# Kernel optimization log

Measured on AMD Instinct MI355X. Metric: run time of the kernel, lower is better.

Reference implementation:

```python
import jax, jax.numpy as jnp
import numpy as np

BN_EPS = 1e-5

def setup_inputs() -> dict:
    key = jax.random.key(0)
    ks = jax.random.split(key, 8)
    N, E, D = 50000, 800000, 128
    x = jax.random.normal(ks[0], (N, D), dtype=jnp.float32)
    edge_index = jax.random.randint(ks[1], (2, E), 0, N, dtype=jnp.int64)
    s = 1.0 / np.sqrt(D)
    W1 = jax.random.uniform(ks[2], (D, D), jnp.float32, -s, s)
    b1 = jax.random.uniform(ks[3], (D,), jnp.float32, -s, s)
    W2 = jax.random.uniform(ks[4], (D, D), jnp.float32, -s, s)
    b2 = jax.random.uniform(ks[5], (D,), jnp.float32, -s, s)
    g1 = jnp.ones((D,), jnp.float32); be1 = jnp.zeros((D,), jnp.float32)
    g2 = jnp.ones((D,), jnp.float32); be2 = jnp.zeros((D,), jnp.float32)
    eps = jnp.zeros((), jnp.float32)  # learnable GIN epsilon (train_eps=True)
    return {"x": x, "edge_index": edge_index, "eps": eps,
            "W1": W1, "b1": b1, "g1": g1, "be1": be1,
            "W2": W2, "b2": b2, "g2": g2, "be2": be2}

def _batchnorm(h, gamma, beta):
    # training-mode BatchNorm1d over node axis (biased variance)
    mu = jnp.mean(h, axis=0)
    var = jnp.mean(jnp.square(h - mu), axis=0)
    return (h - mu) * jax.lax.rsqrt(var + BN_EPS) * gamma + beta

def reference(x, edge_index, eps, W1, b1, g1, be1, W2, b2, g2, be2):
    N = x.shape[0]
    src, dst = edge_index[0], edge_index[1]
    # GIN aggregation: sum of neighbor features (scatter-add to target nodes)
    agg = jax.ops.segment_sum(x[src], dst, num_segments=N)  # [N, D]
    h = (1.0 + eps) * x + agg
    # MLP: Linear -> BN -> ReLU -> Linear
    h = h @ W1.T + b1
    h = jax.nn.relu(_batchnorm(h, g1, be1))
    h = h @ W2.T + b2
    # outer BatchNorm + ReLU
    return jax.nn.relu(_batchnorm(h, g2, be2))
```

## Files before the change

### kernel.cpp

```cpp
#include <hip/hip_runtime.h>
#include <hip/hip_bf16.h>


#define DIM 128
#define SUB 2
#define CAP 32
#define KMAX 64
#define RBLK 2048

typedef unsigned short u16;
typedef __attribute__((ext_vector_type(8))) short short8;
typedef __attribute__((ext_vector_type(8))) unsigned short ushort8;
typedef __attribute__((ext_vector_type(4))) float f32x4;

__device__ inline u16 f2b(float f) {
  unsigned int u = __builtin_bit_cast(unsigned int, f);
  u += 0x7fffu + ((u >> 16) & 1u);
  return (u16)(u >> 16);
}
__device__ inline float b2f(u16 b) {
  unsigned int u = ((unsigned int)b) << 16;
  return __builtin_bit_cast(float, u);
}

__global__ __launch_bounds__(256) void setup_kernel(
    const float* __restrict__ W1, const float* __restrict__ W2,
    int* __restrict__ cursor, u16* __restrict__ wb1, u16* __restrict__ wb2, int ZC) {
  int i = blockIdx.x * 256 + threadIdx.x;
  const int stride = gridDim.x * 256;
  const int e1 = ZC + 4096, e2 = ZC + 8192;
  for (; i < e2; i += stride) {
    if (i < ZC) {
      int4 z = {0, 0, 0, 0};
      reinterpret_cast<int4*>(cursor)[i] = z;
    } else if (i < e1) {
      const int j = i - ZC;
      const float4 v = reinterpret_cast<const float4*>(W1)[j];
      ushort4 o = {f2b(v.x), f2b(v.y), f2b(v.z), f2b(v.w)};
      reinterpret_cast<ushort4*>(wb1)[j] = o;
    } else {
      const int j = i - e1;
      const float4 v = reinterpret_cast<const float4*>(W2)[j];
      ushort4 o = {f2b(v.x), f2b(v.y), f2b(v.z), f2b(v.w)};
      reinterpret_cast<ushort4*>(wb2)[j] = o;
    }
  }
}

__global__ __launch_bounds__(256) void reorder_gemmy_kernel(
    const float* __restrict__ x, const int* __restrict__ ei, const u16* __restrict__ wb1,
    int* __restrict__ cursor, u16* __restrict__ buckets, u16* __restrict__ yb,
    int E, float p8N, int N, int GB) {
  const int bid = blockIdx.x;
  if (bid < GB) {
    const int lane = threadIdx.x & 63;
    const int wid = threadIdx.x >> 6;
    const int l15 = lane & 15;
    const int lg = lane >> 4;
    const int wrow = bid * 64 + wid * 16;

    f32x4 acc[8];
#pragma unroll
    for (int ni = 0; ni < 8; ++ni) acc[ni] = (f32x4){0.f, 0.f, 0.f, 0.f};

    int arow = wrow + l15;
    if (arow >= N) arow = N - 1;

#pragma unroll
    for (int kb = 0; kb < 4; ++kb) {
      const int k0 = kb * 32 + lg * 8;
      const f32x4* A = reinterpret_cast<const f32x4*>(x + (size_t)arow * DIM + k0);
      const f32x4 v0 = __builtin_nontemporal_load(A);
      const f32x4 v1 = __builtin_nontemporal_load(A + 1);
      short8 a;
      a[0] = (short)f2b(v0.x); a[1] = (short)f2b(v0.y);
      a[2] = (short)f2b(v0.z); a[3] = (short)f2b(v0.w);
      a[4] = (short)f2b(v1.x); a[5] = (short)f2b(v1.y);
      a[6] = (short)f2b(v1.z); a[7] = (short)f2b(v1.w);
#pragma unroll
      for (int ni = 0; ni < 8; ++ni) {
        const short8 b = *reinterpret_cast<const short8*>(wb1 + (ni * 16 + l15) * DIM + k0);
        acc[ni] = __builtin_amdgcn_mfma_f32_16x16x32_bf16(a, b, acc[ni], 0, 0, 0);
      }
    }
    const int rbase = wrow + lg * 4;
#pragma unroll
    for (int ni = 0; ni < 8; ++ni) {
      const int col = ni * 16 + l15;
#pragma unroll
      for (int r = 0; r < 4; ++r) {
        const int row = rbase + r;
        if (row < N) yb[(size_t)row * DIM + col] = f2b(acc[ni][r]);
      }
    }
  } else {
    const int rb = bid - GB;
    const int part = rb & 7;
    const int slice = rb >> 3;
    const int perE = (E + 255) >> 8;
    const int beg = slice * perE;
    const int end = min(E, beg + perE);
    const int way = threadIdx.x & 1;
    for (int e = beg + (int)threadIdx.x; e < end; e += 256) {
      const int d = __builtin_nontemporal_load(ei + E + e);
      int p = (int)((float)d * p8N);
      if (p > 7) p = 7;
      if (p != part) continue;
      const int s = __builtin_nontemporal_load(ei + e);
      const int pos = atomicAdd(&cursor[d * SUB + way], 1);
      if (pos < CAP) buckets[d * KMAX + way * CAP + pos] = (u16)s;
    }
  }
}

__global__ __launch_bounds__(256) void aggregate_kernel(
    const u16* __restrict__ yb, const int* __restrict__ cursor,
    const u16* __restrict__ buckets, const float* __restrict__ epsp,
    const float* __restrict__ b1, float* __restrict__ h1, int N) {
  const int wid = threadIdx.x >> 6;
  const int lane = threadIdx.x & 63;
  const int node = blockIdx.x * 4 + wid;
  if (node >= N) return;
  const int slot = lane >> 4;
  const int chunk = lane & 15;
  int c0 = cursor[node * SUB + 0]; if (c0 > CAP) c0 = CAP;
  int c1 = cursor[node * SUB + 1]; if (c1 > CAP) c1 = CAP;
  const int deg = c0 + c1;
  const u16* bk = buckets + node * KMAX;

  int my = 0;
  if (lane < c0) my = bk[lane];
  else if (lane - c0 < c1) my = bk[CAP + lane - c0];

  float acc[8];
#pragma unroll
  for (int f = 0; f < 8; ++f) acc[f] = 0.f;

  for (int t0 = 0; t0 < deg; t0 += 8) {
    const int i1 = t0 + slot;
    const int i2 = t0 + 4 + slot;
    const int s1 = __shfl(my, i1);
    const int s2 = __shfl(my, i2);
    const ushort8 v1 = *reinterpret_cast<const ushort8*>(yb + (size_t)s1 * DIM + chunk * 8);
    const ushort8 v2 = *reinterpret_cast<const ushort8*>(yb + (size_t)s2 * DIM + chunk * 8);
    if (i1 < deg) {
#pragma unroll
      for (int f = 0; f < 8; ++f) acc[f] += b2f(v1[f]);
    }
    if (i2 < deg) {
#pragma unroll
      for (int f = 0; f < 8; ++f) acc[f] += b2f(v2[f]);
    }
  }
#pragma unroll
  for (int f = 0; f < 8; ++f) {
    acc[f] += __shfl_xor(acc[f], 16);
    acc[f] += __shfl_xor(acc[f], 32);
  }
  if (slot == 0) {
    const float k = 1.0f + epsp[0];
    const ushort8 xv = *reinterpret_cast<const ushort8*>(yb + (size_t)node * DIM + chunk * 8);
    const float4 bb0 = *reinterpret_cast<const float4*>(b1 + chunk * 8);
    const float4 bb1 = *reinterpret_cast<const float4*>(b1 + chunk * 8 + 4);
    float4 o0, o1;
    o0.x = acc[0] + k * b2f(xv[0]) + bb0.x;
    o0.y = acc[1] + k * b2f(xv[1]) + bb0.y;
    o0.z = acc[2] + k * b2f(xv[2]) + bb0.z;
    o0.w = acc[3] + k * b2f(xv[3]) + bb0.w;
    o1.x = acc[4] + k * b2f(xv[4]) + bb1.x;
    o1.y = acc[5] + k * b2f(xv[5]) + bb1.y;
    o1.z = acc[6] + k * b2f(xv[6]) + bb1.z;
    o1.w = acc[7] + k * b2f(xv[7]) + bb1.w;
    float4* dst = reinterpret_cast<float4*>(h1 + (size_t)node * DIM + chunk * 8);
    dst[0] = o0;
    dst[1] = o1;
  }
}

__global__ __launch_bounds__(256) void stats_kernel(
    const float* __restrict__ H, float* __restrict__ stats, int N) {
  __shared__ float red[256];
  const int col = threadIdx.x & 127;
  const int sub = threadIdx.x >> 7;
  float s = 0.f, sq = 0.f;
  for (int row = blockIdx.x * 2 + sub; row < N; row += gridDim.x * 2) {
    const float v = H[(size_t)row * DIM + col];
    s += v;
    sq = fmaf(v, v, sq);
  }
  red[threadIdx.x] = s;
  __syncthreads();
  if (sub == 0) unsafeAtomicAdd(&stats[col], s + red[threadIdx.x + 128]);
  __syncthreads();
  red[threadIdx.x] = sq;
  __syncthreads();
  if (sub == 0) unsafeAtomicAdd(&stats[DIM + col], sq + red[threadIdx.x + 128]);
}

__global__ __launch_bounds__(256) void gemm2_kernel(
    const float* __restrict__ A, const u16* __restrict__ Wb,
    const float* __restrict__ bias, const float* __restrict__ statsIn,
    const float* __restrict__ gamma, const float* __restrict__ beta,
    u16* __restrict__ C, float* __restrict__ statsOut, int N, float Ninv) {
  __shared__ float sred[4][DIM];
  __shared__ float qred[4][DIM];
  __shared__ float ssc[DIM];
  __shared__ float ssh[DIM];
  {
    const int t = threadIdx.x;
    if (t < DIM) {
      const float mu = statsIn[t] * Ninv;
      const float var = statsIn[DIM + t] * Ninv - mu * mu;
      const float sc = gamma[t] * rsqrtf(var + 1e-5f);
      ssc[t] = sc;
      ssh[t] = beta[t] - mu * sc;
    }
    __syncthreads();
  }
  const int lane = threadIdx.x & 63;
  const int wid = threadIdx.x >> 6;
  const int l15 = lane & 15;
  const int lg = lane >> 4;
  const int wrow = blockIdx.x * 64 + wid * 16;

  f32x4 acc[8];
#pragma unroll
  for (int ni = 0; ni < 8; ++ni) acc[ni] = (f32x4){0.f, 0.f, 0.f, 0.f};

  int arow = wrow + l15;
  if (arow >= N) arow = N - 1;

#pragma unroll
  for (int kb = 0; kb < 4; ++kb) {
    const int k0 = kb * 32 + lg * 8;
    const float* Ap = A + (size_t)arow * DIM + k0;
    const float4 v0 = *reinterpret_cast<const float4*>(Ap);
    const float4 v1 = *reinterpret_cast<const float4*>(Ap + 4);
    short8 a;
    a[0] = (short)f2b(fmaxf(fmaf(v0.x, ssc[k0 + 0], ssh[k0 + 0]), 0.f));
    a[1] = (short)f2b(fmaxf(fmaf(v0.y, ssc[k0 + 1], ssh[k0 + 1]), 0.f));
    a[2] = (short)f2b(fmaxf(fmaf(v0.z, ssc[k0 + 2], ssh[k0 + 2]), 0.f));
    a[3] = (short)f2b(fmaxf(fmaf(v0.w, ssc[k0 + 3], ssh[k0 + 3]), 0.f));
    a[4] = (short)f2b(fmaxf(fmaf(v1.x, ssc[k0 + 4], ssh[k0 + 4]), 0.f));
    a[5] = (short)f2b(fmaxf(fmaf(v1.y, ssc[k0 + 5], ssh[k0 + 5]), 0.f));
    a[6] = (short)f2b(fmaxf(fmaf(v1.z, ssc[k0 + 6], ssh[k0 + 6]), 0.f));
    a[7] = (short)f2b(fmaxf(fmaf(v1.w, ssc[k0 + 7], ssh[k0 + 7]), 0.f));
#pragma unroll
    for (int ni = 0; ni < 8; ++ni) {
      const short8 b = *reinterpret_cast<const short8*>(Wb + (ni * 16 + l15) * DIM + k0);
      acc[ni] = __builtin_amdgcn_mfma_f32_16x16x32_bf16(a, b, acc[ni], 0, 0, 0);
    }
  }

  const int rbase = wrow + lg * 4;
#pragma unroll
  for (int ni = 0; ni < 8; ++ni) {
    const int col = ni * 16 + l15;
    const float bv = bias[col];
    float s = 0.f, q = 0.f;
#pragma unroll
    for (int r = 0; r < 4; ++r) {
      const int row = rbase + r;
      if (row < N) {
        const float v = acc[ni][r] + bv;
        const u16 bb = f2b(v);
        const float vr = b2f(bb);
        C[(size_t)row * DIM + col] = bb;
        s += vr;
        q = fmaf(vr, vr, q);
      }
    }
    s += __shfl_xor(s, 16); s += __shfl_xor(s, 32);
    q += __shfl_xor(q, 16); q += __shfl_xor(q, 32);
    if (lg == 0) { sred[wid][col] = s; qred[wid][col] = q; }
  }
  __syncthreads();
  const int t = threadIdx.x;
  if (t < DIM) {
    unsafeAtomicAdd(&statsOut[t], sred[0][t] + sred[1][t] + sred[2][t] + sred[3][t]);
  } else {
    const int c = t - DIM;
    unsafeAtomicAdd(&statsOut[DIM + c], qred[0][c] + qred[1][c] + qred[2][c] + qred[3][c]);
  }
}

__global__ __launch_bounds__(256) void bnrelu_kernel(
    const u16* __restrict__ hb, float* __restrict__ out,
    const float* __restrict__ stats, const float* __restrict__ gamma,
    const float* __restrict__ beta, float Ninv, int total8) {
  __shared__ float ssc[DIM];
  __shared__ float ssh[DIM];
  {
    const int t = threadIdx.x;
    if (t < DIM) {
      const float mu = stats[t] * Ninv;
      const float var = stats[DIM + t] * Ninv - mu * mu;
      const float sc = gamma[t] * rsqrtf(var + 1e-5f);
      ssc[t] = sc;
      ssh[t] = beta[t] - mu * sc;
    }
    __syncthreads();
  }
  int i = blockIdx.x * blockDim.x + threadIdx.x;
  const int stride = gridDim.x * blockDim.x;
  for (; i < total8; i += stride) {
    const int c0 = (i * 8) & (DIM - 1);
    const ushort8 v = reinterpret_cast<const ushort8*>(hb)[i];
    f32x4 o0, o1;
    o0.x = fmaxf(fmaf(b2f(v[0]), ssc[c0 + 0], ssh[c0 + 0]), 0.f);
    o0.y = fmaxf(fmaf(b2f(v[1]), ssc[c0 + 1], ssh[c0 + 1]), 0.f);
    o0.z = fmaxf(fmaf(b2f(v[2]), ssc[c0 + 2], ssh[c0 + 2]), 0.f);
    o0.w = fmaxf(fmaf(b2f(v[3]), ssc[c0 + 3], ssh[c0 + 3]), 0.f);
    o1.x = fmaxf(fmaf(b2f(v[4]), ssc[c0 + 4], ssh[c0 + 4]), 0.f);
    o1.y = fmaxf(fmaf(b2f(v[5]), ssc[c0 + 5], ssh[c0 + 5]), 0.f);
    o1.z = fmaxf(fmaf(b2f(v[6]), ssc[c0 + 6], ssh[c0 + 6]), 0.f);
    o1.w = fmaxf(fmaf(b2f(v[7]), ssc[c0 + 7], ssh[c0 + 7]), 0.f);
    __builtin_nontemporal_store(o0, reinterpret_cast<f32x4*>(out) + i * 2);
    __builtin_nontemporal_store(o1, reinterpret_cast<f32x4*>(out) + i * 2 + 1);
  }
}

extern "C" void kernel_launch(void* const* d_in, const int* in_sizes, int n_in,
                              void* d_out, int out_size, void* d_ws, size_t ws_size,
                              hipStream_t stream) {
  const float* x   = (const float*)d_in[0];
  const int*   ei  = (const int*)d_in[1];
  const float* eps = (const float*)d_in[2];
  const float* W1  = (const float*)d_in[3];
  const float* b1  = (const float*)d_in[4];
  const float* g1  = (const float*)d_in[5];
  const float* be1 = (const float*)d_in[6];
  const float* W2  = (const float*)d_in[7];
  const float* b2  = (const float*)d_in[8];
  const float* g2  = (const float*)d_in[9];
  const float* be2 = (const float*)d_in[10];
  float* out = (float*)d_out;

  const int N = in_sizes[0] / DIM;
  const int E = in_sizes[1] / 2;

  u16* yb      = (u16*)d_ws;
  u16* wb1     = yb + (size_t)N * DIM;
  u16* wb2     = wb1 + DIM * DIM;
  u16* buckets = wb2 + DIM * DIM;
  int* cursor  = (int*)(buckets + (size_t)N * KMAX);
  float* stats1 = (float*)(cursor + SUB * N);
  float* stats2 = stats1 + 256;

  float* h1 = (float*)d_out;

  const int ZC = (SUB * N + 512 + 3) / 4;
  const float Ninv = 1.0f / N;
  const float p8N = 8.0f / N;
  const int GB = (N + 63) / 64;

  setup_kernel<<<132, 256, 0, stream>>>(W1, W2, cursor, wb1, wb2, ZC);
  reorder_gemmy_kernel<<<GB + RBLK, 256, 0, stream>>>(
      x, ei, wb1, cursor, buckets, yb, E, p8N, N, GB);
  aggregate_kernel<<<(N + 3) / 4, 256, 0, stream>>>(yb, cursor, buckets, eps, b1, h1, N);
  stats_kernel<<<512, 256, 0, stream>>>(h1, stats1, N);
  gemm2_kernel<<<GB, 256, 0, stream>>>(h1, wb2, b2, stats1, g1, be1, yb, stats2, N, Ninv);
  bnrelu_kernel<<<2048, 256, 0, stream>>>(yb, out, stats2, g2, be2, Ninv, N * (DIM / 8));
}
```

Baseline: 277.0 us.

## Split fused reorder/GEMM kernel into separate launches and preload A rows

Splits the combined edge-bucketing and first-GEMM kernel into two separate kernel launches, removing the block-index branching that shared one grid between them. Both GEMM kernels now issue all eight float4 loads of each row up front, before the bf16 conversion and MFMA loop, so memory latency can overlap. The x loads in the first GEMM also switch from nontemporal to ordinary loads. In exchange, the reorder and GEMM work no longer run concurrently within one grid, and an extra launch is added.

```diff
diff --git a/kernel.cpp b/kernel.cpp
--- a/kernel.cpp
+++ b/kernel.cpp
@@ -47,68 +47,72 @@
   }
 }
 
-__global__ __launch_bounds__(256) void reorder_gemmy_kernel(
-    const float* __restrict__ x, const int* __restrict__ ei, const u16* __restrict__ wb1,
-    int* __restrict__ cursor, u16* __restrict__ buckets, u16* __restrict__ yb,
-    int E, float p8N, int N, int GB) {
-  const int bid = blockIdx.x;
-  if (bid < GB) {
-    const int lane = threadIdx.x & 63;
-    const int wid = threadIdx.x >> 6;
-    const int l15 = lane & 15;
-    const int lg = lane >> 4;
-    const int wrow = bid * 64 + wid * 16;
-
-    f32x4 acc[8];
-#pragma unroll
-    for (int ni = 0; ni < 8; ++ni) acc[ni] = (f32x4){0.f, 0.f, 0.f, 0.f};
-
-    int arow = wrow + l15;
-    if (arow >= N) arow = N - 1;
-
-#pragma unroll
-    for (int kb = 0; kb < 4; ++kb) {
-      const int k0 = kb * 32 + lg * 8;
-      const f32x4* A = reinterpret_cast<const f32x4*>(x + (size_t)arow * DIM + k0);
-      const f32x4 v0 = __builtin_nontemporal_load(A);
-      const f32x4 v1 = __builtin_nontemporal_load(A + 1);
-      short8 a;
-      a[0] = (short)f2b(v0.x); a[1] = (short)f2b(v0.y);
-      a[2] = (short)f2b(v0.z); a[3] = (short)f2b(v0.w);
-      a[4] = (short)f2b(v1.x); a[5] = (short)f2b(v1.y);
-      a[6] = (short)f2b(v1.z); a[7] = (short)f2b(v1.w);
-#pragma unroll
-      for (int ni = 0; ni < 8; ++ni) {
-        const short8 b = *reinterpret_cast<const short8*>(wb1 + (ni * 16 + l15) * DIM + k0);
-        acc[ni] = __builtin_amdgcn_mfma_f32_16x16x32_bf16(a, b, acc[ni], 0, 0, 0);
-      }
-    }
-    const int rbase = wrow + lg * 4;
+__global__ __launch_bounds__(256) void reorder_kernel(
+    const int* __restrict__ ei, int* __restrict__ cursor, u16* __restrict__ buckets,
+    int E, float p8N) {
+  const int part = blockIdx.x & 7;
+  const int slice = blockIdx.x >> 3;
+  const int perE = (E + 255) >> 8;
+  const int beg = slice * perE;
+  const int end = min(E, beg + perE);
+  const int way = threadIdx.x & 1;
+  for (int e = beg + (int)threadIdx.x; e < end; e += 256) {
+    const int d = __builtin_nontemporal_load(ei + E + e);
+    int p = (int)((float)d * p8N);
+    if (p > 7) p = 7;
+    if (p != part) continue;
+    const int s = __builtin_nontemporal_load(ei + e);
+    const int pos = atomicAdd(&cursor[d * SUB + way], 1);
+    if (pos < CAP) buckets[d * KMAX + way * CAP + pos] = (u16)s;
+  }
+}
+
+__global__ __launch_bounds__(256) void gemmy_kernel(
+    const float* __restrict__ x, const u16* __restrict__ Wb,
+    u16* __restrict__ yb, int N) {
+  const int lane = threadIdx.x & 63;
+  const int wid = threadIdx.x >> 6;
+  const int l15 = lane & 15;
+  const int lg = lane >> 4;
+  const int wrow = blockIdx.x * 64 + wid * 16;
+
+  f32x4 acc[8];
+#pragma unroll
+  for (int ni = 0; ni < 8; ++ni) acc[ni] = (f32x4){0.f, 0.f, 0.f, 0.f};
+
+  int arow = wrow + l15;
+  if (arow >= N) arow = N - 1;
+
+  float4 av[8];
+#pragma unroll
+  for (int kb = 0; kb < 4; ++kb) {
+    const float* Ap = x + (size_t)arow * DIM + kb * 32 + lg * 8;
+    av[kb * 2] = *reinterpret_cast<const float4*>(Ap);
+    av[kb * 2 + 1] = *reinterpret_cast<const float4*>(Ap + 4);
+  }
+#pragma unroll
+  for (int kb = 0; kb < 4; ++kb) {
+    const int k0 = kb * 32 + lg * 8;
+    const float4 v0 = av[kb * 2], v1 = av[kb * 2 + 1];
+    short8 a;
+    a[0] = (short)f2b(v0.x); a[1] = (short)f2b(v0.y);
+    a[2] = (short)f2b(v0.z); a[3] = (short)f2b(v0.w);
+    a[4] = (short)f2b(v1.x); a[5] = (short)f2b(v1.y);
+    a[6] = (short)f2b(v1.z); a[7] = (short)f2b(v1.w);
 #pragma unroll
     for (int ni = 0; ni < 8; ++ni) {
-      const int col = ni * 16 + l15;
-#pragma unroll
-      for (int r = 0; r < 4; ++r) {
-        const int row = rbase + r;
-        if (row < N) yb[(size_t)row * DIM + col] = f2b(acc[ni][r]);
-      }
-    }
-  } else {
-    const int rb = bid - GB;
-    const int part = rb & 7;
-    const int slice = rb >> 3;
-    const int perE = (E + 255) >> 8;
-    const int beg = slice * perE;
-    const int end = min(E, beg + perE);
-    const int way = threadIdx.x & 1;
-    for (int e = beg + (int)threadIdx.x; e < end; e += 256) {
-      const int d = __builtin_nontemporal_load(ei + E + e);
-      int p = (int)((float)d * p8N);
-      if (p > 7) p = 7;
-      if (p != part) continue;
-      const int s = __builtin_nontemporal_load(ei + e);
-      const int pos = atomicAdd(&cursor[d * SUB + way], 1);
-      if (pos < CAP) buckets[d * KMAX + way * CAP + pos] = (u16)s;
+      const short8 b = *reinterpret_cast<const short8*>(Wb + (ni * 16 + l15) * DIM + k0);
+      acc[ni] = __builtin_amdgcn_mfma_f32_16x16x32_bf16(a, b, acc[ni], 0, 0, 0);
+    }
+  }
+  const int rbase = wrow + lg * 4;
+#pragma unroll
+  for (int ni = 0; ni < 8; ++ni) {
+    const int col = ni * 16 + l15;
+#pragma unroll
+    for (int r = 0; r < 4; ++r) {
+      const int row = rbase + r;
+      if (row < N) yb[(size_t)row * DIM + col] = f2b(acc[ni][r]);
     }
   }
 }
@@ -230,12 +234,17 @@
   int arow = wrow + l15;
   if (arow >= N) arow = N - 1;
 
+  float4 av[8];
+#pragma unroll
+  for (int kb = 0; kb < 4; ++kb) {
+    const float* Ap = A + (size_t)arow * DIM + kb * 32 + lg * 8;
+    av[kb * 2] = *reinterpret_cast<const float4*>(Ap);
+    av[kb * 2 + 1] = *reinterpret_cast<const float4*>(Ap + 4);
+  }
 #pragma unroll
   for (int kb = 0; kb < 4; ++kb) {
     const int k0 = kb * 32 + lg * 8;
-    const float* Ap = A + (size_t)arow * DIM + k0;
-    const float4 v0 = *reinterpret_cast<const float4*>(Ap);
-    const float4 v1 = *reinterpret_cast<const float4*>(Ap + 4);
+    const float4 v0 = av[kb * 2], v1 = av[kb * 2 + 1];
     short8 a;
     a[0] = (short)f2b(fmaxf(fmaf(v0.x, ssc[k0 + 0], ssh[k0 + 0]), 0.f));
     a[1] = (short)f2b(fmaxf(fmaf(v0.y, ssc[k0 + 1], ssh[k0 + 1]), 0.f));
@@ -355,8 +364,8 @@
   const int GB = (N + 63) / 64;
 
   setup_kernel<<<132, 256, 0, stream>>>(W1, W2, cursor, wb1, wb2, ZC);
-  reorder_gemmy_kernel<<<GB + RBLK, 256, 0, stream>>>(
-      x, ei, wb1, cursor, buckets, yb, E, p8N, N, GB);
+  reorder_kernel<<<RBLK, 256, 0, stream>>>(ei, cursor, buckets, E, p8N);
+  gemmy_kernel<<<GB, 256, 0, stream>>>(x, wb1, yb, N);
   aggregate_kernel<<<(N + 3) / 4, 256, 0, stream>>>(yb, cursor, buckets, eps, b1, h1, N);
   stats_kernel<<<512, 256, 0, stream>>>(h1, stats1, N);
   gemm2_kernel<<<GB, 256, 0, stream>>>(h1, wb2, b2, stats1, g1, be1, yb, stats2, N, Ninv);
```

New measurement: 260.2 us. 1.06x faster.
